# Kernel tuning notes

Hardware: AMD Instinct MI355X
Metric: run time of the kernel (lower is better)

Reference implementation:

```python
import jax, jax.numpy as jnp
import numpy as np

H = 4
N = 1024
E = 4096
LE = 16384
FN = 128
FE = 64
FNO = 128
FEO = 64


def _lin(x, W, b):
    # torch nn.Linear: y = x @ W.T + b, W is [out, in]
    return x @ W.T + b


def setup_inputs() -> dict:
    key = jax.random.key(0)
    ks = jax.random.split(key, 24)
    s = 0.05
    inp = {}
    inp["node_inputs"] = jax.random.normal(ks[0], (N, FN), jnp.float32)
    inp["edge_inputs"] = jax.random.normal(ks[1], (E, FE), jnp.float32)
    inp["src"] = jax.random.randint(ks[2], (E,), 0, N, jnp.int32)
    inp["dst"] = jax.random.randint(ks[3], (E,), 0, N, jnp.int32)
    inp["lg_src"] = jax.random.randint(ks[4], (LE,), 0, E, jnp.int32)
    inp["lg_dst"] = jax.random.randint(ks[5], (LE,), 0, E, jnp.int32)
    # projection linear weights (torch Linear layout [out, in])
    inp["nqW"] = jax.random.normal(ks[6], (H * FN, FN), jnp.float32) * s
    inp["nqb"] = jax.random.normal(ks[7], (H * FN,), jnp.float32) * s
    inp["nkW"] = jax.random.normal(ks[8], (H, FN), jnp.float32) * s
    inp["nkb"] = jax.random.normal(ks[9], (H,), jnp.float32) * s
    inp["nvW"] = jax.random.normal(ks[10], (H * FN, FN), jnp.float32) * s
    inp["nvb"] = jax.random.normal(ks[11], (H * FN,), jnp.float32) * s
    inp["eqW"] = jax.random.normal(ks[12], (H * FE, FE), jnp.float32) * s
    inp["eqb"] = jax.random.normal(ks[13], (H * FE,), jnp.float32) * s
    inp["ekW"] = jax.random.normal(ks[14], (H, FE), jnp.float32) * s
    inp["ekb"] = jax.random.normal(ks[15], (H,), jnp.float32) * s
    inp["evW"] = jax.random.normal(ks[16], (H * FE, FE), jnp.float32) * s
    inp["evb"] = jax.random.normal(ks[17], (H * FE,), jnp.float32) * s
    # convolution output linears
    inp["ncW"] = jax.random.normal(ks[18], (FNO, FN), jnp.float32) * s
    inp["ncb"] = jax.random.normal(ks[19], (FNO,), jnp.float32) * s
    inp["ecW"] = jax.random.normal(ks[20], (FEO, FE), jnp.float32) * s
    inp["ecb"] = jax.random.normal(ks[21], (FEO,), jnp.float32) * s
    return inp


def reference(node_inputs, edge_inputs, src, dst, lg_src, lg_dst,
              nqW, nqb, nkW, nkb, nvW, nvb,
              eqW, eqb, ekW, ekb, evW, evb,
              ncW, ncb, ecW, ecb):
    n, fn = node_inputs.shape
    e, fe = edge_inputs.shape
    # per-head Q/K/V projections; .view(H, -1, F) == row-major reshape
    nq = _lin(node_inputs, nqW, nqb).reshape(H, -1, fn)   # [H,N,FN]
    nk = _lin(node_inputs, nkW, nkb).reshape(H, -1, 1)    # [H,N,1]
    nv = _lin(node_inputs, nvW, nvb).reshape(H, -1, fn)   # [H,N,FN]
    eq = _lin(edge_inputs, eqW, eqb).reshape(H, -1, fe)   # [H,E,FE]
    ek = _lin(edge_inputs, ekW, ekb).reshape(H, -1, 1)    # [H,E,1]
    ev = _lin(edge_inputs, evW, evb).reshape(H, -1, fe)   # [H,E,FE]
    # self attention: softmax(Q @ Q^T @ K, dim=1); associate as Q @ (Q^T K)
    node_sa = jax.nn.softmax(nq @ (jnp.swapaxes(nq, -1, -2) @ nk), axis=1)  # [H,N,1]
    edge_sa = jax.nn.softmax(eq @ (jnp.swapaxes(eq, -1, -2) @ ek), axis=1)  # [H,E,1]
    # vectorized edge-indexed scatter of attention scores into dense projections
    node_proj = jnp.zeros((H, n, n), node_inputs.dtype).at[:, src, dst].set(edge_sa[:, :, 0])
    conn = dst[lg_src]  # g.find_edges(source)[1]: destination node of edge lg_src
    edge_proj = jnp.zeros((H, e, e), edge_inputs.dtype).at[:, lg_src, lg_dst].set(node_sa[:, conn, 0])
    # dense adjacency matrices
    A = jnp.zeros((n, n), node_inputs.dtype).at[src, dst].set(1.0)
    Alg = jnp.zeros((e, e), edge_inputs.dtype).at[lg_src, lg_dst].set(1.0)
    # 'sum' aggregation: (attn_proj * A) @ value, then Linear + relu
    node_out = jax.nn.relu(_lin((node_proj * A) @ nv, ncW, ncb))   # [H,N,FNO]
    edge_out = jax.nn.relu(_lin((edge_proj * Alg) @ ev, ecW, ecb)) # [H,E,FEO]
    return (node_out, edge_out)
```

## Files before the change

### kernel.cpp

```cpp
#include <hip/hip_runtime.h>

#define H_ 4
#define N_ 1024
#define E_ 4096
#define LE_ 16384
#define FN_ 128
#define FE_ 64
#define HTN_ 16384
#define HTE_ 65536
#define CAP_ 32

struct P {
  const float *Xn, *Xe;
  const int *src, *dst, *lgs, *lgd;
  const float *nqW, *nqb, *nkW, *nkb, *nvW, *nvb;
  const float *eqW, *eqb, *ekW, *ekb, *evW, *evb;
  const float *ncW, *ncb, *ecW, *ecb;
  float *out;
  float *NV, *EV, *NK, *EK, *nsa, *esa, *nagg, *eagg;
  int *hkN, *hvN, *hkE, *hvE;
  int *cntN, *cntE, *listN, *listE;
};

__device__ __forceinline__ unsigned hashN(int key) {
  return (((unsigned)key * 2654435761u) >> 16) & (HTN_ - 1);
}
__device__ __forceinline__ unsigned hashE(int key) {
  return (((unsigned)key * 2654435761u) >> 16) & (HTE_ - 1);
}

template<int K, bool RELU>
__device__ void gemm_tile(const float* __restrict__ X, const float* __restrict__ W,
                          const float* __restrict__ b, float* __restrict__ C,
                          int O, int r0, int o0, float* smem, int t) {
  float* Xs = smem;
  float* Ws = smem + 2048;
  const int tn = t & 15, tm = t >> 4;
  float acc[4][4] = {};
  for (int k0 = 0; k0 < K; k0 += 32) {
#pragma unroll
    for (int ph = 0; ph < 2; ++ph) {
      int i4 = t + ph * 256;
      int m = i4 >> 3;
      int k4 = (i4 & 7) << 2;
      int m4 = m >> 2, ml = m & 3;
      float4 vx = *(const float4*)&X[(r0 + m) * K + k0 + k4];
      float4 vw = *(const float4*)&W[(o0 + m) * K + k0 + k4];
      Xs[(k4 + 0) * 64 + ((m4 ^ ((k4 + 0) & 15)) << 2) + ml] = vx.x;
      Xs[(k4 + 1) * 64 + ((m4 ^ ((k4 + 1) & 15)) << 2) + ml] = vx.y;
      Xs[(k4 + 2) * 64 + ((m4 ^ ((k4 + 2) & 15)) << 2) + ml] = vx.z;
      Xs[(k4 + 3) * 64 + ((m4 ^ ((k4 + 3) & 15)) << 2) + ml] = vx.w;
      Ws[(k4 + 0) * 64 + ((m4 ^ ((k4 + 0) & 15)) << 2) + ml] = vw.x;
      Ws[(k4 + 1) * 64 + ((m4 ^ ((k4 + 1) & 15)) << 2) + ml] = vw.y;
      Ws[(k4 + 2) * 64 + ((m4 ^ ((k4 + 2) & 15)) << 2) + ml] = vw.z;
      Ws[(k4 + 3) * 64 + ((m4 ^ ((k4 + 3) & 15)) << 2) + ml] = vw.w;
    }
    __syncthreads();
#pragma unroll
    for (int k = 0; k < 32; ++k) {
      float4 a = *(const float4*)&Xs[k * 64 + ((tm ^ (k & 15)) << 2)];
      float4 b4 = *(const float4*)&Ws[k * 64 + ((tn ^ (k & 15)) << 2)];
      acc[0][0] += a.x * b4.x; acc[0][1] += a.x * b4.y; acc[0][2] += a.x * b4.z; acc[0][3] += a.x * b4.w;
      acc[1][0] += a.y * b4.x; acc[1][1] += a.y * b4.y; acc[1][2] += a.y * b4.z; acc[1][3] += a.y * b4.w;
      acc[2][0] += a.z * b4.x; acc[2][1] += a.z * b4.y; acc[2][2] += a.z * b4.z; acc[2][3] += a.z * b4.w;
      acc[3][0] += a.w * b4.x; acc[3][1] += a.w * b4.y; acc[3][2] += a.w * b4.z; acc[3][3] += a.w * b4.w;
    }
    __syncthreads();
  }
  float4 bv = *(const float4*)&b[o0 + tn * 4];
#pragma unroll
  for (int i = 0; i < 4; ++i) {
    float4 o;
    o.x = acc[i][0] + bv.x; o.y = acc[i][1] + bv.y;
    o.z = acc[i][2] + bv.z; o.w = acc[i][3] + bv.w;
    if (RELU) {
      o.x = fmaxf(o.x, 0.f); o.y = fmaxf(o.y, 0.f);
      o.z = fmaxf(o.z, 0.f); o.w = fmaxf(o.w, 0.f);
    }
    *(float4*)&C[(r0 + tm * 4 + i) * O + o0 + tn * 4] = o;
  }
}

__global__ __launch_bounds__(256) void k1_prep(P p) {
  __shared__ float smem[4096];
  const int t = threadIdx.x, bid = blockIdx.x;
  if (bid < 128) {
    gemm_tile<128, false>(p.Xn, p.nvW, p.nvb, p.NV, 512, (bid >> 3) * 64, (bid & 7) * 64, smem, t);
  } else if (bid < 384) {
    int T2 = bid - 128;
    gemm_tile<64, false>(p.Xe, p.evW, p.evb, p.EV, 256, (T2 >> 2) * 64, (T2 & 3) * 64, smem, t);
  } else {
    int lane = (bid - 384) * 256 + t;
    int4 m4 = make_int4(-1, -1, -1, -1);
    int4* hb = (int4*)p.hkN;
    for (int i = lane; i < 163840 / 4; i += 16384) hb[i] = m4;
    if (lane < N_ + E_) {
      if (lane < N_) p.cntN[lane] = 0;
      else p.cntE[lane - N_] = 0;
    }
    for (int idx = lane; idx < N_ * H_ + E_ * H_; idx += 16384) {
      if (idx < N_ * H_) {
        int r = idx >> 2, o = idx & 3;
        const float4* x4 = (const float4*)(p.Xn + r * FN_);
        const float4* w4 = (const float4*)(p.nkW + o * FN_);
        float acc = p.nkb[o];
        for (int k = 0; k < 32; ++k) {
          float4 x = x4[k], w = w4[k];
          acc += x.x * w.x + x.y * w.y + x.z * w.z + x.w * w.w;
        }
        p.NK[idx] = acc;
      } else {
        int j = idx - N_ * H_;
        int r = j >> 2, o = j & 3;
        const float4* x4 = (const float4*)(p.Xe + r * FE_);
        const float4* w4 = (const float4*)(p.ekW + o * FE_);
        float acc = p.ekb[o];
        for (int k = 0; k < 16; ++k) {
          float4 x = x4[k], w = w4[k];
          acc += x.x * w.x + x.y * w.y + x.z * w.z + x.w * w.w;
        }
        p.EK[j] = acc;
      }
    }
  }
}

__global__ __launch_bounds__(1024) void k2_attn(P p) {
  __shared__ float4 accs[1024];
  __shared__ float red[1024];
  __shared__ float ys[512];
  __shared__ float ts[128];
  __shared__ float zs[4 * 132];
  __shared__ float ds[4], sig[4];
  const int tid = threadIdx.x;

  if (blockIdx.x >= 8) {
    int idx = (blockIdx.x - 8) * 1024 + tid;
    if (idx < E_) {
      int key = p.src[idx] * N_ + p.dst[idx];
      unsigned slot = hashN(key);
      while (true) {
        int prev = atomicCAS(&p.hkN[slot], -1, key);
        if (prev == -1 || prev == key) break;
        slot = (slot + 1) & (HTN_ - 1);
      }
      atomicMax(&p.hvN[slot], idx);
    } else if (idx < E_ + LE_) {
      int l = idx - E_;
      int key = p.lgs[l] * E_ + p.lgd[l];
      unsigned slot = hashE(key);
      while (true) {
        int prev = atomicCAS(&p.hkE[slot], -1, key);
        if (prev == -1 || prev == key) break;
        slot = (slot + 1) & (HTE_ - 1);
      }
      atomicMax(&p.hvE[slot], l);
    }
    return;
  }

  if (blockIdx.x < 4) {
    const int h = blockIdx.x;
    const int r0 = h * 256;
    {
      int g = tid & 127, q = tid >> 7;
      float a0 = 0, a1 = 0, a2 = 0, a3 = 0;
      for (int jj = 0; jj < 32; ++jj) {
        int r = r0 + q * 32 + jj;
        float x = p.Xn[r * FN_ + g];
        float4 k = ((const float4*)p.NK)[r];
        a0 += x * k.x; a1 += x * k.y; a2 += x * k.z; a3 += x * k.w;
      }
      accs[tid] = make_float4(a0, a1, a2, a3);
    }
    __syncthreads();
    for (int off = 512; off >= 128; off >>= 1) {
      if (tid < off) {
        float4 a = accs[tid], b = accs[tid + off];
        accs[tid] = make_float4(a.x + b.x, a.y + b.y, a.z + b.z, a.w + b.w);
      }
      __syncthreads();
    }
    if (tid < 128) {
      float4 a = accs[tid];
      ys[tid * 4 + 0] = a.x; ys[tid * 4 + 1] = a.y;
      ys[tid * 4 + 2] = a.z; ys[tid * 4 + 3] = a.w;
    }
    if (tid >= 128 && tid < 160) {
      int t2 = tid - 128, c = t2 & 3, part = t2 >> 2;
      float s = 0.f;
      for (int j = 0; j < 32; ++j) s += p.NK[(r0 + part * 32 + j) * 4 + c];
      red[t2] = s;
    }
    __syncthreads();
    if (tid < 4) { float s = 0.f; for (int q = 0; q < 8; ++q) s += red[q * 4 + tid]; sig[tid] = s; }
    __syncthreads();
    if (tid < 512) {
      const float4* w4 = (const float4*)(p.nqW + tid * FN_);
      int c = tid >> 7;
      float s = 0.f;
      for (int g4 = 0; g4 < 32; ++g4) {
        float4 w = w4[g4];
        s += w.x * ys[(g4 * 4 + 0) * 4 + c] + w.y * ys[(g4 * 4 + 1) * 4 + c]
           + w.z * ys[(g4 * 4 + 2) * 4 + c] + w.w * ys[(g4 * 4 + 3) * 4 + c];
      }
      red[tid] = s;
    }
    __syncthreads();
    if (tid < 128) {
      float s = red[tid] + red[128 + tid] + red[256 + tid] + red[384 + tid];
      float bb = 0.f;
      for (int c = 0; c < 4; ++c) bb += p.nqb[c * 128 + tid] * sig[c];
      ts[tid] = s + bb;
    }
    __syncthreads();
    if (tid < 512) {
      int c = tid >> 7, g = tid & 127;
      float s = 0.f;
      for (int f = 0; f < 128; ++f) s += p.nqW[(c * 128 + f) * 128 + g] * ts[f];
      zs[c * 132 + g] = s;
    }
    if (tid >= 512 && tid < 516) {
      int c = tid - 512;
      float s = 0.f;
      for (int f = 0; f < 128; ++f) s += p.nqb[c * 128 + f] * ts[f];
      ds[c] = s;
    }
    __syncthreads();
    float sc;
    {
      int c = tid & 3, j = tid >> 2;
      const float4* x4 = (const float4*)(p.Xn + (r0 + j) * FN_);
      const float* z = zs + c * 132;
      float s = ds[c];
      for (int g4 = 0; g4 < 32; ++g4) {
        float4 x = x4[g4];
        s += x.x * z[g4 * 4] + x.y * z[g4 * 4 + 1] + x.z * z[g4 * 4 + 2] + x.w * z[g4 * 4 + 3];
      }
      sc = s;
    }
    red[tid] = sc;
    __syncthreads();
    for (int off = 512; off > 0; off >>= 1) {
      if (tid < off) red[tid] = fmaxf(red[tid], red[tid + off]);
      __syncthreads();
    }
    float m = red[0];
    __syncthreads();
    float e = expf(sc - m);
    red[tid] = e;
    __syncthreads();
    for (int off = 512; off > 0; off >>= 1) {
      if (tid < off) red[tid] += red[tid + off];
      __syncthreads();
    }
    p.nsa[h * N_ + tid] = e / red[0];
  } else {
    const int h = blockIdx.x - 4;
    const int r0 = h * 1024;
    {
      int g = tid & 63, q = tid >> 6;
      float a0 = 0, a1 = 0, a2 = 0, a3 = 0;
      for (int jj = 0; jj < 64; ++jj) {
        int r = r0 + q * 64 + jj;
        float x = p.Xe[r * FE_ + g];
        float4 k = ((const float4*)p.EK)[r];
        a0 += x * k.x; a1 += x * k.y; a2 += x * k.z; a3 += x * k.w;
      }
      accs[tid] = make_float4(a0, a1, a2, a3);
    }
    __syncthreads();
    for (int off = 512; off >= 64; off >>= 1) {
      if (tid < off) {
        float4 a = accs[tid], b = accs[tid + off];
        accs[tid] = make_float4(a.x + b.x, a.y + b.y, a.z + b.z, a.w + b.w);
      }
      __syncthreads();
    }
    if (tid < 64) {
      float4 a = accs[tid];
      ys[tid * 4 + 0] = a.x; ys[tid * 4 + 1] = a.y;
      ys[tid * 4 + 2] = a.z; ys[tid * 4 + 3] = a.w;
    }
    if (tid >= 128 && tid < 160) {
      int t2 = tid - 128, c = t2 & 3, part = t2 >> 2;
      float s = 0.f;
      for (int j = 0; j < 128; ++j) s += p.EK[(r0 + part * 128 + j) * 4 + c];
      red[t2] = s;
    }
    __syncthreads();
    if (tid < 4) { float s = 0.f; for (int q = 0; q < 8; ++q) s += red[q * 4 + tid]; sig[tid] = s; }
    __syncthreads();
    if (tid < 256) {
      const float4* w4 = (const float4*)(p.eqW + tid * FE_);
      int c = tid >> 6;
      float s = 0.f;
      for (int g4 = 0; g4 < 16; ++g4) {
        float4 w = w4[g4];
        s += w.x * ys[(g4 * 4 + 0) * 4 + c] + w.y * ys[(g4 * 4 + 1) * 4 + c]
           + w.z * ys[(g4 * 4 + 2) * 4 + c] + w.w * ys[(g4 * 4 + 3) * 4 + c];
      }
      red[tid] = s;
    }
    __syncthreads();
    if (tid < 64) {
      float s = red[tid] + red[64 + tid] + red[128 + tid] + red[192 + tid];
      float bb = 0.f;
      for (int c = 0; c < 4; ++c) bb += p.eqb[c * 64 + tid] * sig[c];
      ts[tid] = s + bb;
    }
    __syncthreads();
    if (tid < 256) {
      int c = tid >> 6, g = tid & 63;
      float s = 0.f;
      for (int f = 0; f < 64; ++f) s += p.eqW[(c * 64 + f) * 64 + g] * ts[f];
      zs[c * 132 + g] = s;
    }
    if (tid >= 256 && tid < 260) {
      int c = tid - 256;
      float s = 0.f;
      for (int f = 0; f < 64; ++f) s += p.eqb[c * 64 + f] * ts[f];
      ds[c] = s;
    }
    __syncthreads();
    float s4[4];
    {
      const float4* x4 = (const float4*)(p.Xe + (r0 + tid) * FE_);
      s4[0] = ds[0]; s4[1] = ds[1]; s4[2] = ds[2]; s4[3] = ds[3];
      for (int g4 = 0; g4 < 16; ++g4) {
        float4 x = x4[g4];
#pragma unroll
        for (int c = 0; c < 4; ++c) {
          const float* z = zs + c * 132 + g4 * 4;
          s4[c] += x.x * z[0] + x.y * z[1] + x.z * z[2] + x.w * z[3];
        }
      }
    }
    float lm = fmaxf(fmaxf(s4[0], s4[1]), fmaxf(s4[2], s4[3]));
    red[tid] = lm;
    __syncthreads();
    for (int off = 512; off > 0; off >>= 1) {
      if (tid < off) red[tid] = fmaxf(red[tid], red[tid + off]);
      __syncthreads();
    }
    float m = red[0];
    __syncthreads();
    float e0 = expf(s4[0] - m), e1 = expf(s4[1] - m);
    float e2 = expf(s4[2] - m), e3 = expf(s4[3] - m);
    red[tid] = e0 + e1 + e2 + e3;
    __syncthreads();
    for (int off = 512; off > 0; off >>= 1) {
      if (tid < off) red[tid] += red[tid + off];
      __syncthreads();
    }
    float inv = 1.f / red[0];
    ((float4*)(p.esa + h * E_))[tid] = make_float4(e0 * inv, e1 * inv, e2 * inv, e3 * inv);
  }
}

__global__ __launch_bounds__(256) void k3_build(P p) {
  int idx = blockIdx.x * 256 + threadIdx.x;
  if (idx < E_) {
    int e = idx;
    int s = p.src[e], d = p.dst[e];
    int key = s * N_ + d;
    unsigned slot = hashN(key);
    while (p.hkN[slot] != key) slot = (slot + 1) & (HTN_ - 1);
    if (p.hvN[slot] != e) return;
    int pos = atomicAdd(&p.cntN[s], 1) & (CAP_ - 1);
    p.listN[s * CAP_ + pos] = (d << 12) | e;
  } else {
    int l = idx - E_;
    int j = p.lgs[l], c = p.lgd[l];
    int key = j * E_ + c;
    unsigned slot = hashE(key);
    while (p.hkE[slot] != key) slot = (slot + 1) & (HTE_ - 1);
    if (p.hvE[slot] != l) return;
    int pos = atomicAdd(&p.cntE[j], 1) & (CAP_ - 1);
    p.listE[j * CAP_ + pos] = c;
  }
}

__global__ __launch_bounds__(256) void k5_gather(P p) {
  int idx = blockIdx.x * 256 + threadIdx.x;
  if (idx < N_ * 32) {
    int s = idx >> 5, f4 = idx & 31;
    int deg = min(p.cntN[s], CAP_);
    float4 acc[H_];
#pragma unroll
    for (int h = 0; h < H_; ++h) acc[h] = make_float4(0.f, 0.f, 0.f, 0.f);
    for (int i = 0; i < deg; ++i) {
      int pk = p.listN[s * CAP_ + i];
      int e = pk & (E_ - 1), d = pk >> 12;
#pragma unroll
      for (int h = 0; h < H_; ++h) {
        float a = p.esa[h * E_ + e];
        float4 v = ((const float4*)(p.NV + h * (N_ * FN_) + d * FN_))[f4];
        acc[h].x += a * v.x; acc[h].y += a * v.y;
        acc[h].z += a * v.z; acc[h].w += a * v.w;
      }
    }
#pragma unroll
    for (int h = 0; h < H_; ++h)
      ((float4*)(p.nagg + h * (N_ * FN_) + s * FN_))[f4] = acc[h];
  } else {
    idx -= N_ * 32;
    int j = idx >> 4, f4 = idx & 15;
    int deg = min(p.cntE[j], CAP_);
    float4 acc[H_];
#pragma unroll
    for (int h = 0; h < H_; ++h) acc[h] = make_float4(0.f, 0.f, 0.f, 0.f);
    for (int i = 0; i < deg; ++i) {
      int c = p.listE[j * CAP_ + i];
#pragma unroll
      for (int h = 0; h < H_; ++h) {
        float4 v = ((const float4*)(p.EV + h * (E_ * FE_) + c * FE_))[f4];
        acc[h].x += v.x; acc[h].y += v.y; acc[h].z += v.z; acc[h].w += v.w;
      }
    }
    int cn = p.dst[j];
#pragma unroll
    for (int h = 0; h < H_; ++h) {
      float a = p.nsa[h * N_ + cn];
      ((float4*)(p.eagg + h * (E_ * FE_) + j * FE_))[f4] =
          make_float4(a * acc[h].x, a * acc[h].y, a * acc[h].z, a * acc[h].w);
    }
  }
}

__global__ __launch_bounds__(256) void k4_out(P p) {
  __shared__ float smem[4096];
  const int t = threadIdx.x, bid = blockIdx.x;
  if (bid < 128)
    gemm_tile<128, true>(p.nagg, p.ncW, p.ncb, p.out, 128, (bid >> 1) * 64, (bid & 1) * 64, smem, t);
  else {
    int T2 = bid - 128;
    gemm_tile<64, true>(p.eagg, p.ecW, p.ecb, p.out + (size_t)H_ * N_ * 128, 64, T2 * 64, 0, smem, t);
  }
}

extern "C" void kernel_launch(void* const* d_in, const int* in_sizes, int n_in,
                              void* d_out, int out_size, void* d_ws, size_t ws_size,
                              hipStream_t stream) {
  P p;
  p.Xn  = (const float*)d_in[0];
  p.Xe  = (const float*)d_in[1];
  p.src = (const int*)d_in[2];
  p.dst = (const int*)d_in[3];
  p.lgs = (const int*)d_in[4];
  p.lgd = (const int*)d_in[5];
  p.nqW = (const float*)d_in[6];  p.nqb = (const float*)d_in[7];
  p.nkW = (const float*)d_in[8];  p.nkb = (const float*)d_in[9];
  p.nvW = (const float*)d_in[10]; p.nvb = (const float*)d_in[11];
  p.eqW = (const float*)d_in[12]; p.eqb = (const float*)d_in[13];
  p.ekW = (const float*)d_in[14]; p.ekb = (const float*)d_in[15];
  p.evW = (const float*)d_in[16]; p.evb = (const float*)d_in[17];
  p.ncW = (const float*)d_in[18]; p.ncb = (const float*)d_in[19];
  p.ecW = (const float*)d_in[20]; p.ecb = (const float*)d_in[21];
  p.out = (float*)d_out;

  float* f = (float*)d_ws;
  p.NV   = f; f += N_ * H_ * FN_;
  p.EV   = f; f += E_ * H_ * FE_;
  p.NK   = f; f += N_ * H_;
  p.EK   = f; f += E_ * H_;
  p.nsa  = f; f += H_ * N_;
  p.esa  = f; f += H_ * E_;
  p.nagg = f; f += H_ * N_ * FN_;
  p.eagg = f; f += H_ * E_ * FE_;
  p.hkN  = (int*)f; f += HTN_;
  p.hvN  = (int*)f; f += HTN_;
  p.hkE  = (int*)f; f += HTE_;
  p.hvE  = (int*)f; f += HTE_;
  p.cntN = (int*)f; f += N_;
  p.cntE = (int*)f; f += E_;
  p.listN = (int*)f; f += N_ * CAP_;
  p.listE = (int*)f; f += E_ * CAP_;

  k1_prep<<<448, 256, 0, stream>>>(p);
  k2_attn<<<28, 1024, 0, stream>>>(p);
  k3_build<<<80, 256, 0, stream>>>(p);
  k5_gather<<<384, 256, 0, stream>>>(p);
  k4_out<<<384, 256, 0, stream>>>(p);
}
```

Before: 164.4 us.

## Fuse prep into attention kernel and gather into output GEMM, drop intermediates

Merges the value-projection GEMMs and the key projections into the attention kernel: keys are computed per block into shared memory instead of being written to global scratch. The neighbour gather is fused with the output linear so the aggregated features go straight into swizzled shared memory, which removes the nagg/eagg round trips through global memory. Hash-table and counter initialisation moves to hipMemsetAsync calls, and the launch count drops from five kernels to three. In exchange, the 1024-thread GEMM blocks pack four 256-thread sub-tiles and pad with dummy syncthreads, which can lower occupancy and complicate the barrier logic.

```diff
diff --git a/kernel.cpp b/kernel.cpp
--- a/kernel.cpp
+++ b/kernel.cpp
@@ -17,7 +17,7 @@
   const float *eqW, *eqb, *ekW, *ekb, *evW, *evb;
   const float *ncW, *ncb, *ecW, *ecb;
   float *out;
-  float *NV, *EV, *NK, *EK, *nsa, *esa, *nagg, *eagg;
+  float *NV, *EV, *nsa, *esa;
   int *hkN, *hvN, *hkE, *hvE;
   int *cntN, *cntE, *listN, *listE;
 };
@@ -81,61 +81,30 @@
   }
 }
 
-__global__ __launch_bounds__(256) void k1_prep(P p) {
-  __shared__ float smem[4096];
-  const int t = threadIdx.x, bid = blockIdx.x;
-  if (bid < 128) {
-    gemm_tile<128, false>(p.Xn, p.nvW, p.nvb, p.NV, 512, (bid >> 3) * 64, (bid & 7) * 64, smem, t);
-  } else if (bid < 384) {
-    int T2 = bid - 128;
-    gemm_tile<64, false>(p.Xe, p.evW, p.evb, p.EV, 256, (T2 >> 2) * 64, (T2 & 3) * 64, smem, t);
-  } else {
-    int lane = (bid - 384) * 256 + t;
-    int4 m4 = make_int4(-1, -1, -1, -1);
-    int4* hb = (int4*)p.hkN;
-    for (int i = lane; i < 163840 / 4; i += 16384) hb[i] = m4;
-    if (lane < N_ + E_) {
-      if (lane < N_) p.cntN[lane] = 0;
-      else p.cntE[lane - N_] = 0;
-    }
-    for (int idx = lane; idx < N_ * H_ + E_ * H_; idx += 16384) {
-      if (idx < N_ * H_) {
-        int r = idx >> 2, o = idx & 3;
-        const float4* x4 = (const float4*)(p.Xn + r * FN_);
-        const float4* w4 = (const float4*)(p.nkW + o * FN_);
-        float acc = p.nkb[o];
-        for (int k = 0; k < 32; ++k) {
-          float4 x = x4[k], w = w4[k];
-          acc += x.x * w.x + x.y * w.y + x.z * w.z + x.w * w.w;
-        }
-        p.NK[idx] = acc;
-      } else {
-        int j = idx - N_ * H_;
-        int r = j >> 2, o = j & 3;
-        const float4* x4 = (const float4*)(p.Xe + r * FE_);
-        const float4* w4 = (const float4*)(p.ekW + o * FE_);
-        float acc = p.ekb[o];
-        for (int k = 0; k < 16; ++k) {
-          float4 x = x4[k], w = w4[k];
-          acc += x.x * w.x + x.y * w.y + x.z * w.z + x.w * w.w;
-        }
-        p.EK[j] = acc;
-      }
-    }
-  }
-}
-
-__global__ __launch_bounds__(1024) void k2_attn(P p) {
-  __shared__ float4 accs[1024];
-  __shared__ float red[1024];
-  __shared__ float ys[512];
-  __shared__ float ts[128];
-  __shared__ float zs[4 * 132];
-  __shared__ float ds[4], sig[4];
+__global__ __launch_bounds__(1024) void kA(P p) {
+  __shared__ float smem[16384];
   const int tid = threadIdx.x;
-
-  if (blockIdx.x >= 8) {
-    int idx = (blockIdx.x - 8) * 1024 + tid;
+  const int bid = blockIdx.x;
+
+  if (bid >= 28) {
+    const int gg = (bid - 28) * 4 + (tid >> 8);
+    const int ts_ = tid & 255;
+    float* gsm = smem + (tid >> 8) * 4096;
+    if (gg % 3 == 0) {
+      const int tile = gg / 3;
+      gemm_tile<128, false>(p.Xn, p.nvW, p.nvb, p.NV, 512,
+                            (tile >> 3) * 64, (tile & 7) * 64, gsm, ts_);
+    } else {
+      const int tile = gg - gg / 3 - 1;
+      gemm_tile<64, false>(p.Xe, p.evW, p.evb, p.EV, 256,
+                           (tile >> 2) * 64, (tile & 3) * 64, gsm, ts_);
+      __syncthreads(); __syncthreads(); __syncthreads(); __syncthreads();
+    }
+    return;
+  }
+
+  if (bid >= 8) {
+    int idx = (bid - 8) * 1024 + tid;
     if (idx < E_) {
       int key = p.src[idx] * N_ + p.dst[idx];
       unsigned slot = hashN(key);
@@ -159,16 +128,41 @@
     return;
   }
 
-  if (blockIdx.x < 4) {
-    const int h = blockIdx.x;
+  float4* accs = (float4*)smem;
+  float* red = smem + 4096;
+  float* ys  = smem + 5120;
+  float* ts  = smem + 5632;
+  float* zs  = smem + 5760;
+  float* ds  = smem + 6288;
+  float* sig = smem + 6292;
+  float* Ks  = smem + 6304;
+
+  if (bid < 4) {
+    const int h = bid;
     const int r0 = h * 256;
+    float* wkw = Ks + 1024;
+    for (int i = tid; i < 512; i += 1024) wkw[i] = p.nkW[i];
+    __syncthreads();
+    {
+      const int rl = tid >> 2, c = tid & 3;
+      const float4* x4 = (const float4*)(p.Xn + (r0 + rl) * FN_);
+      const float4* w4 = (const float4*)(wkw + c * FN_);
+      float acc = p.nkb[c];
+      for (int k = 0; k < 32; ++k) {
+        float4 x = x4[k], w = w4[k];
+        acc += x.x * w.x + x.y * w.y + x.z * w.z + x.w * w.w;
+      }
+      Ks[tid] = acc;
+    }
+    __syncthreads();
     {
       int g = tid & 127, q = tid >> 7;
+      const float4* Ks4 = (const float4*)Ks;
       float a0 = 0, a1 = 0, a2 = 0, a3 = 0;
       for (int jj = 0; jj < 32; ++jj) {
-        int r = r0 + q * 32 + jj;
-        float x = p.Xn[r * FN_ + g];
-        float4 k = ((const float4*)p.NK)[r];
+        int lr = q * 32 + jj;
+        float x = p.Xn[(r0 + lr) * FN_ + g];
+        float4 k = Ks4[lr];
         a0 += x * k.x; a1 += x * k.y; a2 += x * k.z; a3 += x * k.w;
       }
       accs[tid] = make_float4(a0, a1, a2, a3);
@@ -189,7 +183,7 @@
     if (tid >= 128 && tid < 160) {
       int t2 = tid - 128, c = t2 & 3, part = t2 >> 2;
       float s = 0.f;
-      for (int j = 0; j < 32; ++j) s += p.NK[(r0 + part * 32 + j) * 4 + c];
+      for (int j = 0; j < 32; ++j) s += Ks[(part * 32 + j) * 4 + c];
       red[t2] = s;
     }
     __syncthreads();
@@ -256,15 +250,38 @@
     }
     p.nsa[h * N_ + tid] = e / red[0];
   } else {
-    const int h = blockIdx.x - 4;
+    const int h = bid - 4;
     const int r0 = h * 1024;
+    float* wkw = Ks + 4096;
+    for (int i = tid; i < 256; i += 1024) wkw[i] = p.ekW[i];
+    __syncthreads();
+    {
+      const float4* x4 = (const float4*)(p.Xe + (r0 + tid) * FE_);
+      const float4* w0 = (const float4*)wkw;
+      const float4* w1 = (const float4*)(wkw + 64);
+      const float4* w2 = (const float4*)(wkw + 128);
+      const float4* w3 = (const float4*)(wkw + 192);
+      float a0 = p.ekb[0], a1 = p.ekb[1], a2 = p.ekb[2], a3 = p.ekb[3];
+      for (int k = 0; k < 16; ++k) {
+        float4 x = x4[k];
+        float4 u0 = w0[k], u1 = w1[k], u2 = w2[k], u3 = w3[k];
+        a0 += x.x * u0.x + x.y * u0.y + x.z * u0.z + x.w * u0.w;
+        a1 += x.x * u1.x + x.y * u1.y + x.z * u1.z + x.w * u1.w;
+        a2 += x.x * u2.x + x.y * u2.y + x.z * u2.z + x.w * u2.w;
+        a3 += x.x * u3.x + x.y * u3.y + x.z * u3.z + x.w * u3.w;
+      }
+      Ks[tid * 4 + 0] = a0; Ks[tid * 4 + 1] = a1;
+      Ks[tid * 4 + 2] = a2; Ks[tid * 4 + 3] = a3;
+    }
+    __syncthreads();
     {
       int g = tid & 63, q = tid >> 6;
+      const float4* Ks4 = (const float4*)Ks;
       float a0 = 0, a1 = 0, a2 = 0, a3 = 0;
       for (int jj = 0; jj < 64; ++jj) {
-        int r = r0 + q * 64 + jj;
-        float x = p.Xe[r * FE_ + g];
-        float4 k = ((const float4*)p.EK)[r];
+        int lr = q * 64 + jj;
+        float x = p.Xe[(r0 + lr) * FE_ + g];
+        float4 k = Ks4[lr];
         a0 += x * k.x; a1 += x * k.y; a2 += x * k.z; a3 += x * k.w;
       }
       accs[tid] = make_float4(a0, a1, a2, a3);
@@ -285,7 +302,7 @@
     if (tid >= 128 && tid < 160) {
       int t2 = tid - 128, c = t2 & 3, part = t2 >> 2;
       float s = 0.f;
-      for (int j = 0; j < 128; ++j) s += p.EK[(r0 + part * 128 + j) * 4 + c];
+      for (int j = 0; j < 128; ++j) s += Ks[(part * 128 + j) * 4 + c];
       red[t2] = s;
     }
     __syncthreads();
@@ -358,7 +375,7 @@
   }
 }
 
-__global__ __launch_bounds__(256) void k3_build(P p) {
+__global__ __launch_bounds__(256) void kB(P p) {
   int idx = blockIdx.x * 256 + threadIdx.x;
   if (idx < E_) {
     int e = idx;
@@ -381,61 +398,147 @@
   }
 }
 
-__global__ __launch_bounds__(256) void k5_gather(P p) {
-  int idx = blockIdx.x * 256 + threadIdx.x;
-  if (idx < N_ * 32) {
-    int s = idx >> 5, f4 = idx & 31;
-    int deg = min(p.cntN[s], CAP_);
-    float4 acc[H_];
-#pragma unroll
-    for (int h = 0; h < H_; ++h) acc[h] = make_float4(0.f, 0.f, 0.f, 0.f);
-    for (int i = 0; i < deg; ++i) {
-      int pk = p.listN[s * CAP_ + i];
-      int e = pk & (E_ - 1), d = pk >> 12;
-#pragma unroll
-      for (int h = 0; h < H_; ++h) {
-        float a = p.esa[h * E_ + e];
-        float4 v = ((const float4*)(p.NV + h * (N_ * FN_) + d * FN_))[f4];
-        acc[h].x += a * v.x; acc[h].y += a * v.y;
-        acc[h].z += a * v.z; acc[h].w += a * v.w;
-      }
-    }
-#pragma unroll
-    for (int h = 0; h < H_; ++h)
-      ((float4*)(p.nagg + h * (N_ * FN_) + s * FN_))[f4] = acc[h];
+__global__ __launch_bounds__(256) void kC(P p) {
+  __shared__ float smem[10240];
+  const int t = threadIdx.x, bid = blockIdx.x;
+  float* Xs = smem;
+  float* Ws = smem + 8192;
+  const int tn = t & 15, tm = t >> 4;
+
+  if (bid < 128) {
+    const int rt = bid >> 1, o0 = (bid & 1) << 6;
+    const int h = rt >> 4, p0 = (rt & 15) << 6;
+    {
+      const int m = t >> 2, q = t & 3;
+      const int s = p0 + m;
+      const int deg = min(p.cntN[s], CAP_);
+      float4 acc[8];
+#pragma unroll
+      for (int f = 0; f < 8; ++f) acc[f] = make_float4(0.f, 0.f, 0.f, 0.f);
+      const float4* NV4 = (const float4*)p.NV + (h << 15);
+      const float* esah = p.esa + h * E_;
+      for (int i = 0; i < deg; ++i) {
+        int pk = p.listN[s * CAP_ + i];
+        int e = pk & (E_ - 1), d = pk >> 12;
+        float a = esah[e];
+        const float4* v4 = NV4 + (d << 5);
+#pragma unroll
+        for (int f = 0; f < 8; ++f) {
+          float4 v = v4[q + (f << 2)];
+          acc[f].x += a * v.x; acc[f].y += a * v.y;
+          acc[f].z += a * v.z; acc[f].w += a * v.w;
+        }
+      }
+      const int m4 = m >> 2, ml = m & 3;
+#pragma unroll
+      for (int f = 0; f < 8; ++f) {
+        int k4 = (q + (f << 2)) << 2;
+        Xs[(k4 + 0) * 64 + ((m4 ^ ((k4 + 0) & 15)) << 2) + ml] = acc[f].x;
+        Xs[(k4 + 1) * 64 + ((m4 ^ ((k4 + 1) & 15)) << 2) + ml] = acc[f].y;
+        Xs[(k4 + 2) * 64 + ((m4 ^ ((k4 + 2) & 15)) << 2) + ml] = acc[f].z;
+        Xs[(k4 + 3) * 64 + ((m4 ^ ((k4 + 3) & 15)) << 2) + ml] = acc[f].w;
+      }
+    }
+    float c16[4][4] = {};
+    for (int k0 = 0; k0 < 128; k0 += 32) {
+#pragma unroll
+      for (int ph = 0; ph < 2; ++ph) {
+        int i4 = t + ph * 256;
+        int mw = i4 >> 3, k4 = (i4 & 7) << 2;
+        int w4i = mw >> 2, wl = mw & 3;
+        float4 vw = *(const float4*)&p.ncW[(o0 + mw) * 128 + k0 + k4];
+        Ws[(k4 + 0) * 64 + ((w4i ^ ((k4 + 0) & 15)) << 2) + wl] = vw.x;
+        Ws[(k4 + 1) * 64 + ((w4i ^ ((k4 + 1) & 15)) << 2) + wl] = vw.y;
+        Ws[(k4 + 2) * 64 + ((w4i ^ ((k4 + 2) & 15)) << 2) + wl] = vw.z;
+        Ws[(k4 + 3) * 64 + ((w4i ^ ((k4 + 3) & 15)) << 2) + wl] = vw.w;
+      }
+      __syncthreads();
+#pragma unroll
+      for (int kk = 0; kk < 32; ++kk) {
+        int k = k0 + kk;
+        float4 a = *(const float4*)&Xs[k * 64 + ((tm ^ (k & 15)) << 2)];
+        float4 b4 = *(const float4*)&Ws[kk * 64 + ((tn ^ (kk & 15)) << 2)];
+        c16[0][0] += a.x * b4.x; c16[0][1] += a.x * b4.y; c16[0][2] += a.x * b4.z; c16[0][3] += a.x * b4.w;
+        c16[1][0] += a.y * b4.x; c16[1][1] += a.y * b4.y; c16[1][2] += a.y * b4.z; c16[1][3] += a.y * b4.w;
+        c16[2][0] += a.z * b4.x; c16[2][1] += a.z * b4.y; c16[2][2] += a.z * b4.z; c16[2][3] += a.z * b4.w;
+        c16[3][0] += a.w * b4.x; c16[3][1] += a.w * b4.y; c16[3][2] += a.w * b4.z; c16[3][3] += a.w * b4.w;
+      }
+      __syncthreads();
+    }
+    float4 bv = *(const float4*)&p.ncb[o0 + tn * 4];
+#pragma unroll
+    for (int i = 0; i < 4; ++i) {
+      float4 o;
+      o.x = fmaxf(c16[i][0] + bv.x, 0.f); o.y = fmaxf(c16[i][1] + bv.y, 0.f);
+      o.z = fmaxf(c16[i][2] + bv.z, 0.f); o.w = fmaxf(c16[i][3] + bv.w, 0.f);
+      *(float4*)&p.out[((h << 10) + p0 + tm * 4 + i) * 128 + o0 + tn * 4] = o;
+    }
   } else {
-    idx -= N_ * 32;
-    int j = idx >> 4, f4 = idx & 15;
-    int deg = min(p.cntE[j], CAP_);
-    float4 acc[H_];
-#pragma unroll
-    for (int h = 0; h < H_; ++h) acc[h] = make_float4(0.f, 0.f, 0.f, 0.f);
-    for (int i = 0; i < deg; ++i) {
-      int c = p.listE[j * CAP_ + i];
-#pragma unroll
-      for (int h = 0; h < H_; ++h) {
-        float4 v = ((const float4*)(p.EV + h * (E_ * FE_) + c * FE_))[f4];
-        acc[h].x += v.x; acc[h].y += v.y; acc[h].z += v.z; acc[h].w += v.w;
-      }
-    }
-    int cn = p.dst[j];
-#pragma unroll
-    for (int h = 0; h < H_; ++h) {
-      float a = p.nsa[h * N_ + cn];
-      ((float4*)(p.eagg + h * (E_ * FE_) + j * FE_))[f4] =
-          make_float4(a * acc[h].x, a * acc[h].y, a * acc[h].z, a * acc[h].w);
-    }
-  }
-}
-
-__global__ __launch_bounds__(256) void k4_out(P p) {
-  __shared__ float smem[4096];
-  const int t = threadIdx.x, bid = blockIdx.x;
-  if (bid < 128)
-    gemm_tile<128, true>(p.nagg, p.ncW, p.ncb, p.out, 128, (bid >> 1) * 64, (bid & 1) * 64, smem, t);
-  else {
-    int T2 = bid - 128;
-    gemm_tile<64, true>(p.eagg, p.ecW, p.ecb, p.out + (size_t)H_ * N_ * 128, 64, T2 * 64, 0, smem, t);
+    const int rt = bid - 128;
+    const int h = rt >> 6, j0 = (rt & 63) << 6;
+    {
+      const int m = t >> 2, q = t & 3;
+      const int j = j0 + m;
+      const int deg = min(p.cntE[j], CAP_);
+      float4 acc[4];
+#pragma unroll
+      for (int f = 0; f < 4; ++f) acc[f] = make_float4(0.f, 0.f, 0.f, 0.f);
+      const float4* EV4 = (const float4*)p.EV + (h << 16);
+      for (int i = 0; i < deg; ++i) {
+        int c = p.listE[j * CAP_ + i];
+        const float4* v4 = EV4 + (c << 4);
+#pragma unroll
+        for (int f = 0; f < 4; ++f) {
+          float4 v = v4[q + (f << 2)];
+          acc[f].x += v.x; acc[f].y += v.y; acc[f].z += v.z; acc[f].w += v.w;
+        }
+      }
+      float a = p.nsa[h * N_ + p.dst[j]];
+      const int m4 = m >> 2, ml = m & 3;
+#pragma unroll
+      for (int f = 0; f < 4; ++f) {
+        int k4 = (q + (f << 2)) << 2;
+        Xs[(k4 + 0) * 64 + ((m4 ^ ((k4 + 0) & 15)) << 2) + ml] = a * acc[f].x;
+        Xs[(k4 + 1) * 64 + ((m4 ^ ((k4 + 1) & 15)) << 2) + ml] = a * acc[f].y;
+        Xs[(k4 + 2) * 64 + ((m4 ^ ((k4 + 2) & 15)) << 2) + ml] = a * acc[f].z;
+        Xs[(k4 + 3) * 64 + ((m4 ^ ((k4 + 3) & 15)) << 2) + ml] = a * acc[f].w;
+      }
+    }
+    float c16[4][4] = {};
+    for (int k0 = 0; k0 < 64; k0 += 32) {
+#pragma unroll
+      for (int ph = 0; ph < 2; ++ph) {
+        int i4 = t + ph * 256;
+        int mw = i4 >> 3, k4 = (i4 & 7) << 2;
+        int w4i = mw >> 2, wl = mw & 3;
+        float4 vw = *(const float4*)&p.ecW[mw * 64 + k0 + k4];
+        Ws[(k4 + 0) * 64 + ((w4i ^ ((k4 + 0) & 15)) << 2) + wl] = vw.x;
+        Ws[(k4 + 1) * 64 + ((w4i ^ ((k4 + 1) & 15)) << 2) + wl] = vw.y;
+        Ws[(k4 + 2) * 64 + ((w4i ^ ((k4 + 2) & 15)) << 2) + wl] = vw.z;
+        Ws[(k4 + 3) * 64 + ((w4i ^ ((k4 + 3) & 15)) << 2) + wl] = vw.w;
+      }
+      __syncthreads();
+#pragma unroll
+      for (int kk = 0; kk < 32; ++kk) {
+        int k = k0 + kk;
+        float4 a = *(const float4*)&Xs[k * 64 + ((tm ^ (k & 15)) << 2)];
+        float4 b4 = *(const float4*)&Ws[kk * 64 + ((tn ^ (kk & 15)) << 2)];
+        c16[0][0] += a.x * b4.x; c16[0][1] += a.x * b4.y; c16[0][2] += a.x * b4.z; c16[0][3] += a.x * b4.w;
+        c16[1][0] += a.y * b4.x; c16[1][1] += a.y * b4.y; c16[1][2] += a.y * b4.z; c16[1][3] += a.y * b4.w;
+        c16[2][0] += a.z * b4.x; c16[2][1] += a.z * b4.y; c16[2][2] += a.z * b4.z; c16[2][3] += a.z * b4.w;
+        c16[3][0] += a.w * b4.x; c16[3][1] += a.w * b4.y; c16[3][2] += a.w * b4.z; c16[3][3] += a.w * b4.w;
+      }
+      __syncthreads();
+    }
+    float4 bv = *(const float4*)&p.ecb[tn * 4];
+    float* out2 = p.out + 524288;
+#pragma unroll
+    for (int i = 0; i < 4; ++i) {
+      float4 o;
+      o.x = fmaxf(c16[i][0] + bv.x, 0.f); o.y = fmaxf(c16[i][1] + bv.y, 0.f);
+      o.z = fmaxf(c16[i][2] + bv.z, 0.f); o.w = fmaxf(c16[i][3] + bv.w, 0.f);
+      *(float4*)&out2[((h << 12) + j0 + tm * 4 + i) * 64 + tn * 4] = o;
+    }
   }
 }
 
@@ -462,24 +565,22 @@
   float* f = (float*)d_ws;
   p.NV   = f; f += N_ * H_ * FN_;
   p.EV   = f; f += E_ * H_ * FE_;
-  p.NK   = f; f += N_ * H_;
-  p.EK   = f; f += E_ * H_;
   p.nsa  = f; f += H_ * N_;
   p.esa  = f; f += H_ * E_;
-  p.nagg = f; f += H_ * N_ * FN_;
-  p.eagg = f; f += H_ * E_ * FE_;
-  p.hkN  = (int*)f; f += HTN_;
-  p.hvN  = (int*)f; f += HTN_;
-  p.hkE  = (int*)f; f += HTE_;
-  p.hvE  = (int*)f; f += HTE_;
-  p.cntN = (int*)f; f += N_;
-  p.cntE = (int*)f; f += E_;
-  p.listN = (int*)f; f += N_ * CAP_;
-  p.listE = (int*)f; f += E_ * CAP_;
-
-  k1_prep<<<448, 256, 0, stream>>>(p);
-  k2_attn<<<28, 1024, 0, stream>>>(p);
-  k3_build<<<80, 256, 0, stream>>>(p);
-  k5_gather<<<384, 256, 0, stream>>>(p);
-  k4_out<<<384, 256, 0, stream>>>(p);
-}
+  int* ip = (int*)f;
+  p.hkN  = ip; ip += HTN_;
+  p.hvN  = ip; ip += HTN_;
+  p.hkE  = ip; ip += HTE_;
+  p.hvE  = ip; ip += HTE_;
+  p.cntN = ip; ip += N_;
+  p.cntE = ip; ip += E_;
+  p.listN = ip; ip += N_ * CAP_;
+  p.listE = ip; ip += E_ * CAP_;
+
+  hipMemsetAsync(p.hkN, 0xFF, (size_t)(2 * HTN_ + 2 * HTE_) * sizeof(int), stream);
+  hipMemsetAsync(p.cntN, 0, (size_t)(N_ + E_) * sizeof(int), stream);
+
+  kA<<<124, 1024, 0, stream>>>(p);
+  kB<<<80, 256, 0, stream>>>(p);
+  kC<<<384, 256, 0, stream>>>(p);
+}
```

Result: faster. 151.6 us (-7.8%).
